# Kernel tuning notes

Hardware: AMD Instinct MI355X
Metric: run time of the kernel (lower is better)

The kernel has to match this reference:

```python
import jax, jax.numpy as jnp
import numpy as np

WS = (7, 7, 7)
DIM = 96
HEADS = 3
NW = 64          # windows per image (mask batch)
BW = 512         # B_ = total windows = 8 images * 64 windows
N = WS[0] * WS[1] * WS[2]  # 343


def _rel_pos_index(ws):
    # Faithful reproduction of the torch buffer (including its multipliers).
    coords = np.stack(np.meshgrid(np.arange(ws[0]), np.arange(ws[1]), np.arange(ws[2]), indexing='ij'))
    cf = coords.reshape(3, -1)                      # [3, N]
    rc = cf[:, :, None] - cf[:, None, :]            # [3, N, N]
    rc = rc.transpose(1, 2, 0).astype(np.int32)     # [N, N, 3]
    rc[:, :, 0] += ws[0] - 1
    rc[:, :, 1] += ws[1] - 1
    rc[:, :, 2] += ws[2] - 1
    rc[:, :, 0] *= 3 * ws[1] - 1
    rc[:, :, 1] *= 2 * ws[1] - 1
    return rc.sum(-1)                               # [N, N]


def setup_inputs() -> dict:
    key = jax.random.key(0)
    ks = jax.random.split(key, 8)
    table_len = (2 * WS[0] - 1) * (2 * WS[1] - 1) * (2 * WS[2] - 1)  # 2197
    x = jax.random.normal(ks[0], (BW, N, DIM), dtype=jnp.float32)
    # shift-window additive mask: 0 where allowed, -100 where masked
    mask = jnp.where(jax.random.uniform(ks[1], (NW, N, N)) < 0.9, 0.0, -100.0).astype(jnp.float32)
    Wqkv = jax.random.normal(ks[2], (3 * DIM, DIM), dtype=jnp.float32) * 0.02
    bqkv = jnp.zeros((3 * DIM,), dtype=jnp.float32)
    Wproj = jax.random.normal(ks[3], (DIM, DIM), dtype=jnp.float32) * 0.02
    bproj = jnp.zeros((DIM,), dtype=jnp.float32)
    logit_scale = jnp.full((HEADS, 1, 1), np.log(10.0), dtype=jnp.float32)
    bias_table = jax.random.normal(ks[4], (table_len, HEADS), dtype=jnp.float32) * 0.02
    rpi = jnp.asarray(_rel_pos_index(WS))           # [N, N] int32
    return {"x": x, "mask": mask, "Wqkv": Wqkv, "bqkv": bqkv,
            "Wproj": Wproj, "bproj": bproj, "logit_scale": logit_scale,
            "bias_table": bias_table, "rpi": rpi}


def reference(x, mask, Wqkv, bqkv, Wproj, bproj, logit_scale, bias_table, rpi):
    B_, Nn, C = x.shape
    H = HEADS
    hd = C // H
    qkv = x @ Wqkv.T + bqkv                          # [B_, N, 3C]
    qkv = qkv.reshape(B_, Nn, 3, H, hd).transpose(2, 0, 3, 1, 4)  # [3, B_, H, N, hd]
    q, k, v = qkv[0], qkv[1], qkv[2]
    # cosine attention: L2-normalize q and k (torch F.normalize, eps=1e-12)
    qn = q / jnp.maximum(jnp.linalg.norm(q, axis=-1, keepdims=True), 1e-12)
    kn = k / jnp.maximum(jnp.linalg.norm(k, axis=-1, keepdims=True), 1e-12)
    attn = jnp.einsum('bhnd,bhmd->bhnm', qn, kn)     # [B_, H, N, N]
    scale = jnp.exp(jnp.minimum(logit_scale, jnp.log(jnp.float32(100.0))))  # [H,1,1]
    attn = attn * scale[None]
    rel_bias = bias_table[rpi.reshape(-1)].reshape(Nn, Nn, H).transpose(2, 0, 1)  # [H, N, N]
    attn = attn + rel_bias[None]
    nW = mask.shape[0]
    attn = attn.reshape(B_ // nW, nW, H, Nn, Nn) + mask[None, :, None]
    attn = attn.reshape(B_, H, Nn, Nn)
    attn = jax.nn.softmax(attn, axis=-1)
    out = jnp.einsum('bhnm,bhmd->bhnd', attn, v)     # [B_, H, N, hd]
    out = out.transpose(0, 2, 1, 3).reshape(B_, Nn, C)
    return out @ Wproj.T + bproj
```

## Files before the change

### kernel.cpp

```cpp
#include <hip/hip_runtime.h>

typedef __attribute__((ext_vector_type(8))) _Float16 half8;
typedef __attribute__((ext_vector_type(4))) _Float16 half4;
typedef __attribute__((ext_vector_type(2))) __fp16 fp16x2;
typedef __attribute__((ext_vector_type(4))) float f32x4;
typedef __attribute__((ext_vector_type(2))) unsigned int uint2v;
typedef __attribute__((ext_vector_type(4))) unsigned int uint4v;

__device__ __forceinline__ _Float16 f2h(float f) { return (_Float16)f; }

#define LOG100 4.605170185988091f
#define LOG2E 1.44269504088896f
#define PADNEG (-100000.0f)

#define MASK_BLOCKS 7744
#define BIAS_BLOCKS 363
__global__ void k_prep(const float* __restrict__ mask, const int* __restrict__ rpi,
                       const float* __restrict__ table,
                       unsigned char* __restrict__ mb, float* __restrict__ bf) {
  if (blockIdx.x < MASK_BLOCKS) {
    int tid = blockIdx.x * 256 + threadIdx.x;
    if (tid >= 64 * 484 * 64) return;
    int lane = tid & 63, idx = tid >> 6;
    int kt = idx % 22, t2 = idx / 22;
    int qt = t2 % 22, w = t2 / 22;
    int R = qt * 16 + (lane & 15), col0 = kt * 16 + (lane >> 4) * 4;
    unsigned bits = 0;
#pragma unroll
    for (int rr = 0; rr < 4; rr++) {
      int col = col0 + rr;
      bool pass = true;
      if (R < 343 && col < 343) pass = mask[((size_t)w * 343 + R) * 343 + col] > -50.f;
      bits |= (pass ? 1u : 0u) << rr;
    }
    mb[tid] = (unsigned char)bits;
  } else {
    int tid = (blockIdx.x - MASK_BLOCKS) * 256 + threadIdx.x;
    if (tid >= 3 * 484 * 64) return;
    int lane = tid & 63, idx = tid >> 6;
    int kt = idx % 22, t2 = idx / 22;
    int qt = t2 % 22, h = t2 / 22;
    int R = qt * 16 + (lane & 15), col0 = kt * 16 + (lane >> 4) * 4;
    f32x4 o;
#pragma unroll
    for (int rr = 0; rr < 4; rr++) {
      int col = col0 + rr;
      o[rr] = (R < 343 && col < 343) ? table[rpi[R * 343 + col] * 3 + h] * LOG2E : PADNEG;
    }
    reinterpret_cast<f32x4*>(bf)[tid] = o;
  }
}

__global__ __launch_bounds__(1024, 1) void k_qkv(
    const float* __restrict__ x, const float* __restrict__ Wqkv,
    const float* __restrict__ bqkv, const float* __restrict__ ls,
    _Float16* __restrict__ q_ws, _Float16* __restrict__ k_ws, _Float16* __restrict__ v_ws) {
  __shared__ alignas(16) _Float16 Wl[288 * 104];
  const int tid = threadIdx.x;
  for (int i = tid; i < 6912; i += 1024) {
    f32x4 w4 = reinterpret_cast<const f32x4*>(Wqkv)[i];
    int f = i * 4, row = f / 96, col = f - row * 96;
    _Float16* dst = &Wl[row * 104 + col];
    dst[0] = f2h(w4[0]); dst[1] = f2h(w4[1]); dst[2] = f2h(w4[2]); dst[3] = f2h(w4[3]);
  }
  __syncthreads();
  const int lane = tid & 63, wv = tid >> 6;
  const int ln15 = lane & 15, quad = lane >> 4;
  const int rowbase = blockIdx.x * 256 + wv * 16;
  const int arow = rowbase + ln15;

  half8 afr[3];
#pragma unroll
  for (int kt = 0; kt < 3; kt++) {
    const float* xp = x + (size_t)arow * 96 + kt * 32 + quad * 8;
    f32x4 a0 = *reinterpret_cast<const f32x4*>(xp);
    f32x4 a1 = *reinterpret_cast<const f32x4*>(xp + 4);
    half8 a;
    a[0] = f2h(a0[0]); a[1] = f2h(a0[1]); a[2] = f2h(a0[2]); a[3] = f2h(a0[3]);
    a[4] = f2h(a1[0]); a[5] = f2h(a1[1]); a[6] = f2h(a1[2]); a[7] = f2h(a1[3]);
    afr[kt] = a;
  }

  int Bb[4], Nn[4];
#pragma unroll
  for (int rr = 0; rr < 4; rr++) {
    int R = rowbase + quad * 4 + rr;
    Bb[rr] = R / 343;
    Nn[rr] = R - Bb[rr] * 343;
  }

  auto ctile = [&](int nt) -> f32x4 {
    f32x4 c = {0.f, 0.f, 0.f, 0.f};
#pragma unroll
    for (int kt = 0; kt < 3; kt++) {
      half8 b = *reinterpret_cast<const half8*>(&Wl[(nt * 16 + ln15) * 104 + kt * 32 + quad * 8]);
      c = __builtin_amdgcn_mfma_f32_16x16x32_f16(afr[kt], b, c, 0, 0, 0);
    }
    return c;
  };

#pragma unroll
  for (int h = 0; h < 3; h++) {
    float sc = __expf(fminf(ls[h], LOG100)) * LOG2E;
    {
      f32x4 c0 = ctile(2 * h), c1 = ctile(2 * h + 1);
      float b0 = bqkv[32 * h + ln15], b1 = bqkv[32 * h + 16 + ln15];
#pragma unroll
      for (int rr = 0; rr < 4; rr++) { c0[rr] += b0; c1[rr] += b1; }
#pragma unroll
      for (int rr = 0; rr < 4; rr++) {
        float s2 = c0[rr] * c0[rr] + c1[rr] * c1[rr];
        s2 += __shfl_xor(s2, 1); s2 += __shfl_xor(s2, 2);
        s2 += __shfl_xor(s2, 4); s2 += __shfl_xor(s2, 8);
        float inv = sc / fmaxf(sqrtf(s2), 1e-12f);
        size_t base = ((size_t)(Bb[rr] * 3 + h) * 343 + Nn[rr]) * 32;
        q_ws[base + ln15] = f2h(c0[rr] * inv);
        q_ws[base + 16 + ln15] = f2h(c1[rr] * inv);
      }
    }
    {
      f32x4 c0 = ctile(6 + 2 * h), c1 = ctile(7 + 2 * h);
      float b0 = bqkv[96 + 32 * h + ln15], b1 = bqkv[96 + 32 * h + 16 + ln15];
#pragma unroll
      for (int rr = 0; rr < 4; rr++) { c0[rr] += b0; c1[rr] += b1; }
#pragma unroll
      for (int rr = 0; rr < 4; rr++) {
        float s2 = c0[rr] * c0[rr] + c1[rr] * c1[rr];
        s2 += __shfl_xor(s2, 1); s2 += __shfl_xor(s2, 2);
        s2 += __shfl_xor(s2, 4); s2 += __shfl_xor(s2, 8);
        float inv = 1.0f / fmaxf(sqrtf(s2), 1e-12f);
        size_t base = ((size_t)(Bb[rr] * 3 + h) * 343 + Nn[rr]) * 32;
        k_ws[base + ln15] = f2h(c0[rr] * inv);
        k_ws[base + 16 + ln15] = f2h(c1[rr] * inv);
      }
    }
    {
      f32x4 c0 = ctile(12 + 2 * h), c1 = ctile(13 + 2 * h);
      float b0 = bqkv[192 + 32 * h + ln15], b1 = bqkv[192 + 32 * h + 16 + ln15];
#pragma unroll
      for (int rr = 0; rr < 4; rr++) {
        size_t base = ((size_t)(Bb[rr] * 3 + h) * 343 + Nn[rr]) * 32;
        v_ws[base + ln15] = f2h(c0[rr] + b0);
        v_ws[base + 16 + ln15] = f2h(c1[rr] + b1);
      }
    }
  }
}

#define KSTR 40
#define VSTR 360
__global__ __launch_bounds__(1024, 8) void k_attn(
    const _Float16* __restrict__ q_ws, const _Float16* __restrict__ k_ws,
    const _Float16* __restrict__ v_ws, const float* __restrict__ bfrag,
    const unsigned char* __restrict__ mb, _Float16* __restrict__ a_ws) {
  __shared__ alignas(16) _Float16 Kl[344 * KSTR];
  __shared__ alignas(16) _Float16 Vt[32 * VSTR];
  const int blk = blockIdx.x;
  const int b = blk / 3, h = blk - b * 3, w = b & 63;
  const size_t slice = (size_t)(b * 3 + h) * 343 * 32;
  const _Float16* qb = q_ws + slice;
  const _Float16* kb = k_ws + slice;
  const _Float16* vb = v_ws + slice;
  const int tid = threadIdx.x, lane = tid & 63, wv = tid >> 6;
  const int ln15 = lane & 15, quad = lane >> 4;

  for (int i = tid; i < 344 * 4; i += 1024) {
    int t = i >> 2, c4 = i & 3;
    half8 kv;
    if (t < 343) kv = *reinterpret_cast<const half8*>(kb + t * 32 + c4 * 8);
    else kv = (half8)(_Float16)0.f;
    *reinterpret_cast<half8*>(&Kl[t * KSTR + c4 * 8]) = kv;
  }
  for (int i = tid; i < 1372; i += 1024) {
    int n = i >> 2, c4 = i & 3;
    half8 vv = *reinterpret_cast<const half8*>(vb + n * 32 + c4 * 8);
#pragma unroll
    for (int j = 0; j < 8; j++) Vt[(c4 * 8 + j) * VSTR + n] = vv[j];
  }
  for (int i = tid; i < 288; i += 1024) {
    int d = i / 9, cc = i - d * 9;
    Vt[d * VSTR + 343 + cc] = (_Float16)0.f;
  }
  __syncthreads();

  const float* bfh = bfrag + (size_t)h * 484 * 64 * 4;
  const unsigned char* mbw = mb + (size_t)w * 484 * 64;
  const fp16x2 kOnes = __builtin_amdgcn_cvt_pkrtz(1.f, 1.f);

#pragma unroll 1
  for (int qt = wv; qt < 22; qt += 16) {
    const int qbase = qt * 16;
    half8 aq = *reinterpret_cast<const half8*>(qb + (size_t)(qbase + ln15) * 32 + quad * 8);
    const f32x4* bq = reinterpret_cast<const f32x4*>(bfh) + (size_t)qt * 22 * 64 + lane;
    const unsigned char* mq = mbw + (size_t)qt * 22 * 64 + lane;

    f32x4 o0 = {0.f, 0.f, 0.f, 0.f}, o1 = {0.f, 0.f, 0.f, 0.f};
    float l00 = 0.f, l01 = 0.f, l10 = 0.f, l11 = 0.f;

    f32x4 ba = bq[0], bb = bq[64];
    unsigned mva = mq[0], mvb = mq[64];
    bq += 128; mq += 128;

#pragma unroll 1
    for (int kc = 0; kc < 11; kc++) {
      int r0 = kc * 32 + ln15;
      int r1 = r0 + 16;
      r1 = (r1 > 343) ? 343 : r1;
      half8 ak0 = *reinterpret_cast<const half8*>(&Kl[r0 * KSTR + quad * 8]);
      half8 ak1 = *reinterpret_cast<const half8*>(&Kl[r1 * KSTR + quad * 8]);
      f32x4 s0 = __builtin_amdgcn_mfma_f32_16x16x32_f16(ak0, aq, ba, 0, 0, 0);
      f32x4 s1 = __builtin_amdgcn_mfma_f32_16x16x32_f16(ak1, aq, bb, 0, 0, 0);

      f32x4 nba = ba, nbb = bb;
      unsigned nmva = mva, nmvb = mvb;
      if (kc < 10) {
        nba = bq[0]; nbb = bq[64];
        nmva = mq[0]; nmvb = mq[64];
        bq += 128; mq += 128;
      }

      float e00 = __builtin_amdgcn_exp2f(s0[0]);
      float e01 = __builtin_amdgcn_exp2f(s0[1]);
      float e02 = __builtin_amdgcn_exp2f(s0[2]);
      float e03 = __builtin_amdgcn_exp2f(s0[3]);
      float e10 = __builtin_amdgcn_exp2f(s1[0]);
      float e11 = __builtin_amdgcn_exp2f(s1[1]);
      float e12 = __builtin_amdgcn_exp2f(s1[2]);
      float e13 = __builtin_amdgcn_exp2f(s1[3]);
      float p00 = ((mva >> 0) & 1u) ? e00 : 0.f;
      float p01 = ((mva >> 1) & 1u) ? e01 : 0.f;
      float p02 = ((mva >> 2) & 1u) ? e02 : 0.f;
      float p03 = ((mva >> 3) & 1u) ? e03 : 0.f;
      float p10 = ((mvb >> 0) & 1u) ? e10 : 0.f;
      float p11 = ((mvb >> 1) & 1u) ? e11 : 0.f;
      float p12 = ((mvb >> 2) & 1u) ? e12 : 0.f;
      float p13 = ((mvb >> 3) & 1u) ? e13 : 0.f;

      fp16x2 w00 = __builtin_amdgcn_cvt_pkrtz(p00, p01);
      fp16x2 w01 = __builtin_amdgcn_cvt_pkrtz(p02, p03);
      fp16x2 w10 = __builtin_amdgcn_cvt_pkrtz(p10, p11);
      fp16x2 w11 = __builtin_amdgcn_cvt_pkrtz(p12, p13);

      l00 = __builtin_amdgcn_fdot2(w00, kOnes, l00, false);
      l01 = __builtin_amdgcn_fdot2(w01, kOnes, l01, false);
      l10 = __builtin_amdgcn_fdot2(w10, kOnes, l10, false);
      l11 = __builtin_amdgcn_fdot2(w11, kOnes, l11, false);

      unsigned a0 = __builtin_bit_cast(unsigned int, w00);
      unsigned a1 = __builtin_bit_cast(unsigned int, w01);
      unsigned b0 = __builtin_bit_cast(unsigned int, w10);
      unsigned b1 = __builtin_bit_cast(unsigned int, w11);
      uint2v r32a = __builtin_amdgcn_permlane32_swap(a0, b0, false, false);
      uint2v r32b = __builtin_amdgcn_permlane32_swap(a1, b1, false, false);
      uint2v r16a = __builtin_amdgcn_permlane16_swap(r32a[0], r32a[1], false, false);
      uint2v r16b = __builtin_amdgcn_permlane16_swap(r32b[0], r32b[1], false, false);
      uint4v pw = {r16a[0], r16b[0], r16a[1], r16b[1]};
      half8 pb = __builtin_bit_cast(half8, pw);

      half8 v0 = *reinterpret_cast<const half8*>(&Vt[ln15 * VSTR + kc * 32 + quad * 8]);
      half8 v1 = *reinterpret_cast<const half8*>(&Vt[(16 + ln15) * VSTR + kc * 32 + quad * 8]);
      o0 = __builtin_amdgcn_mfma_f32_16x16x32_f16(v0, pb, o0, 0, 0, 0);
      o1 = __builtin_amdgcn_mfma_f32_16x16x32_f16(v1, pb, o1, 0, 0, 0);

      ba = nba; bb = nbb; mva = nmva; mvb = nmvb;
    }

    float l = (l00 + l01) + (l10 + l11);
    l += __shfl_xor(l, 16);
    l += __shfl_xor(l, 32);

    const int R = qbase + ln15;
    if (R < 343) {
      float inv = 1.0f / l;
      size_t obase = ((size_t)b * 343 + R) * 96 + h * 32;
      half4 w0, w1;
#pragma unroll
      for (int rr = 0; rr < 4; rr++) {
        w0[rr] = f2h(o0[rr] * inv);
        w1[rr] = f2h(o1[rr] * inv);
      }
      *reinterpret_cast<half4*>(a_ws + obase + quad * 4) = w0;
      *reinterpret_cast<half4*>(a_ws + obase + 16 + quad * 4) = w1;
    }
  }
}

__global__ __launch_bounds__(1024, 1) void k_proj(
    const _Float16* __restrict__ a_ws, const float* __restrict__ Wproj,
    const float* __restrict__ bproj, float* __restrict__ out) {
  __shared__ alignas(16) _Float16 Wl[96 * 104];
  const int tid = threadIdx.x;
  for (int i = tid; i < 2304; i += 1024) {
    f32x4 w4 = reinterpret_cast<const f32x4*>(Wproj)[i];
    int f = i * 4, row = f / 96, col = f - row * 96;
    _Float16* dst = &Wl[row * 104 + col];
    dst[0] = f2h(w4[0]); dst[1] = f2h(w4[1]); dst[2] = f2h(w4[2]); dst[3] = f2h(w4[3]);
  }
  __syncthreads();
  const int lane = tid & 63, wv = tid >> 6;
  const int ln15 = lane & 15, quad = lane >> 4;
  const int rowbase = blockIdx.x * 256 + wv * 16;
  half8 afr[3];
#pragma unroll
  for (int kt = 0; kt < 3; kt++) {
    afr[kt] = *reinterpret_cast<const half8*>(a_ws + (size_t)(rowbase + ln15) * 96 + kt * 32 + quad * 8);
  }
#pragma unroll
  for (int nt = 0; nt < 6; nt++) {
    f32x4 c = {0.f, 0.f, 0.f, 0.f};
#pragma unroll
    for (int kt = 0; kt < 3; kt++) {
      half8 bfr = *reinterpret_cast<const half8*>(&Wl[(nt * 16 + ln15) * 104 + kt * 32 + quad * 8]);
      c = __builtin_amdgcn_mfma_f32_16x16x32_f16(afr[kt], bfr, c, 0, 0, 0);
    }
    float bb = bproj[nt * 16 + ln15];
#pragma unroll
    for (int rr = 0; rr < 4; rr++) {
      int R = rowbase + quad * 4 + rr;
      out[(size_t)R * 96 + nt * 16 + ln15] = c[rr] + bb;
    }
  }
}

extern "C" void kernel_launch(void* const* d_in, const int* in_sizes, int n_in,
                              void* d_out, int out_size, void* d_ws, size_t ws_size,
                              hipStream_t stream) {
  const float* x     = (const float*)d_in[0];
  const float* mask  = (const float*)d_in[1];
  const float* Wqkv  = (const float*)d_in[2];
  const float* bqkv  = (const float*)d_in[3];
  const float* Wproj = (const float*)d_in[4];
  const float* bproj = (const float*)d_in[5];
  const float* ls    = (const float*)d_in[6];
  const float* btab  = (const float*)d_in[7];
  const int*   rpi   = (const int*)d_in[8];
  float* out = (float*)d_out;

  char* ws = (char*)d_ws;
  _Float16* q_ws = (_Float16*)(ws);
  _Float16* k_ws = (_Float16*)(ws + 33718272);
  _Float16* v_ws = (_Float16*)(ws + 67436544);
  _Float16* a_ws = (_Float16*)(ws + 101154816);
  float* bfrag = (float*)(ws + 134873088);
  unsigned char* mbf = (unsigned char*)(ws + 136359936);

  hipLaunchKernelGGL(k_prep, dim3(MASK_BLOCKS + BIAS_BLOCKS), dim3(256), 0, stream,
                     mask, rpi, btab, mbf, bfrag);
  hipLaunchKernelGGL(k_qkv, dim3(686), dim3(1024), 0, stream, x, Wqkv, bqkv, ls, q_ws, k_ws, v_ws);
  hipLaunchKernelGGL(k_attn, dim3(1536), dim3(1024), 0, stream, q_ws, k_ws, v_ws,
                     bfrag, mbf, a_ws);
  hipLaunchKernelGGL(k_proj, dim3(686), dim3(1024), 0, stream, a_ws, Wproj, bproj, out);
}
```

Baseline: 289.7 us.

## Compute softmax row sums via MFMA and precompute fp16 AND-masks for attention

Replaces the per-lane fdot2 row-sum accumulation and cross-lane shuffles with an extra MFMA against a ones matrix, so the denominator comes out already reduced per row. When the workspace is large enough, the prep kernel expands the mask into 16-bit all-ones/zero words laid out per 32-column chunk. A new attention kernel applies the mask with a bitwise AND on packed fp16 probabilities instead of per-element selects. This trades more mask memory traffic (16 bytes per lane per chunk instead of 1 byte) and an extra MFMA per chunk for fewer VALU operations.

```diff
diff --git a/kernel.cpp b/kernel.cpp
--- a/kernel.cpp
+++ b/kernel.cpp
@@ -15,25 +15,53 @@
 
 #define MASK_BLOCKS 7744
 #define BIAS_BLOCKS 363
+#define WS_BIG_END 152219648ull
+
 __global__ void k_prep(const float* __restrict__ mask, const int* __restrict__ rpi,
-                       const float* __restrict__ table,
-                       unsigned char* __restrict__ mb, float* __restrict__ bf) {
+                       const float* __restrict__ table, unsigned char* __restrict__ mb,
+                       uint4v* __restrict__ mand, float* __restrict__ bf, int big) {
   if (blockIdx.x < MASK_BLOCKS) {
-    int tid = blockIdx.x * 256 + threadIdx.x;
-    if (tid >= 64 * 484 * 64) return;
-    int lane = tid & 63, idx = tid >> 6;
-    int kt = idx % 22, t2 = idx / 22;
-    int qt = t2 % 22, w = t2 / 22;
-    int R = qt * 16 + (lane & 15), col0 = kt * 16 + (lane >> 4) * 4;
-    unsigned bits = 0;
-#pragma unroll
-    for (int rr = 0; rr < 4; rr++) {
-      int col = col0 + rr;
-      bool pass = true;
-      if (R < 343 && col < 343) pass = mask[((size_t)w * 343 + R) * 343 + col] > -50.f;
-      bits |= (pass ? 1u : 0u) << rr;
-    }
-    mb[tid] = (unsigned char)bits;
+    if (big) {
+      int tid = blockIdx.x * 256 + threadIdx.x;
+      if (tid >= 64 * 22 * 11 * 64) return;
+      int lane = tid & 63, idx = tid >> 6;
+      int kc = idx % 11, t2 = idx / 11;
+      int qt = t2 % 22, w = t2 / 22;
+      int R = qt * 16 + (lane & 15), col0 = (lane >> 4) * 4;
+      unsigned wd[4];
+#pragma unroll
+      for (int j = 0; j < 2; j++) {
+        int kt = kc * 2 + j;
+        unsigned bits[4];
+#pragma unroll
+        for (int rr = 0; rr < 4; rr++) {
+          int col = kt * 16 + col0 + rr;
+          bool pass = true;
+          if (R < 343 && col < 343) pass = mask[((size_t)w * 343 + R) * 343 + col] > -50.f;
+          bits[rr] = pass ? 0xFFFFu : 0u;
+        }
+        wd[j * 2] = bits[0] | (bits[1] << 16);
+        wd[j * 2 + 1] = bits[2] | (bits[3] << 16);
+      }
+      uint4v o = {wd[0], wd[1], wd[2], wd[3]};
+      mand[tid] = o;
+    } else {
+      int tid = blockIdx.x * 256 + threadIdx.x;
+      if (tid >= 64 * 484 * 64) return;
+      int lane = tid & 63, idx = tid >> 6;
+      int kt = idx % 22, t2 = idx / 22;
+      int qt = t2 % 22, w = t2 / 22;
+      int R = qt * 16 + (lane & 15), col0 = kt * 16 + (lane >> 4) * 4;
+      unsigned bits = 0;
+#pragma unroll
+      for (int rr = 0; rr < 4; rr++) {
+        int col = col0 + rr;
+        bool pass = true;
+        if (R < 343 && col < 343) pass = mask[((size_t)w * 343 + R) * 343 + col] > -50.f;
+        bits |= (pass ? 1u : 0u) << rr;
+      }
+      mb[tid] = (unsigned char)bits;
+    }
   } else {
     int tid = (blockIdx.x - MASK_BLOCKS) * 256 + threadIdx.x;
     if (tid >= 3 * 484 * 64) return;
@@ -149,6 +177,127 @@
 
 #define KSTR 40
 #define VSTR 360
+
+__global__ __launch_bounds__(1024, 8) void k_attn_big(
+    const _Float16* __restrict__ q_ws, const _Float16* __restrict__ k_ws,
+    const _Float16* __restrict__ v_ws, const float* __restrict__ bfrag,
+    const uint4v* __restrict__ mand, _Float16* __restrict__ a_ws) {
+  __shared__ alignas(16) _Float16 Kl[344 * KSTR];
+  __shared__ alignas(16) _Float16 Vt[32 * VSTR];
+  const int blk = blockIdx.x;
+  const int b = blk / 3, h = blk - b * 3, w = b & 63;
+  const size_t slice = (size_t)(b * 3 + h) * 343 * 32;
+  const _Float16* qb = q_ws + slice;
+  const _Float16* kb = k_ws + slice;
+  const _Float16* vb = v_ws + slice;
+  const int tid = threadIdx.x, lane = tid & 63, wv = tid >> 6;
+  const int ln15 = lane & 15, quad = lane >> 4;
+
+  for (int i = tid; i < 344 * 4; i += 1024) {
+    int t = i >> 2, c4 = i & 3;
+    half8 kv;
+    if (t < 343) kv = *reinterpret_cast<const half8*>(kb + t * 32 + c4 * 8);
+    else kv = (half8)(_Float16)0.f;
+    *reinterpret_cast<half8*>(&Kl[t * KSTR + c4 * 8]) = kv;
+  }
+  for (int i = tid; i < 1372; i += 1024) {
+    int n = i >> 2, c4 = i & 3;
+    half8 vv = *reinterpret_cast<const half8*>(vb + n * 32 + c4 * 8);
+#pragma unroll
+    for (int j = 0; j < 8; j++) Vt[(c4 * 8 + j) * VSTR + n] = vv[j];
+  }
+  for (int i = tid; i < 288; i += 1024) {
+    int d = i / 9, cc = i - d * 9;
+    Vt[d * VSTR + 343 + cc] = (_Float16)0.f;
+  }
+  __syncthreads();
+
+  const float* bfh = bfrag + (size_t)h * 484 * 64 * 4;
+  half8 ones8;
+#pragma unroll
+  for (int j = 0; j < 8; j++) ones8[j] = (_Float16)1.f;
+
+#pragma unroll 1
+  for (int qt = wv; qt < 22; qt += 16) {
+    const int qbase = qt * 16;
+    half8 aq = *reinterpret_cast<const half8*>(qb + (size_t)(qbase + ln15) * 32 + quad * 8);
+    const f32x4* bq = reinterpret_cast<const f32x4*>(bfh) + (size_t)qt * 22 * 64 + lane;
+    const uint4v* mq = mand + ((size_t)w * 22 + qt) * 11 * 64 + lane;
+
+    f32x4 o0 = {0.f, 0.f, 0.f, 0.f}, o1 = {0.f, 0.f, 0.f, 0.f};
+    f32x4 lacc = {0.f, 0.f, 0.f, 0.f};
+
+    f32x4 ba = bq[0], bb = bq[64];
+    uint4v mw = mq[0];
+    bq += 128; mq += 64;
+
+#pragma unroll 1
+    for (int kc = 0; kc < 11; kc++) {
+      int r0 = kc * 32 + ln15;
+      int r1 = r0 + 16;
+      r1 = (r1 > 343) ? 343 : r1;
+      half8 ak0 = *reinterpret_cast<const half8*>(&Kl[r0 * KSTR + quad * 8]);
+      half8 ak1 = *reinterpret_cast<const half8*>(&Kl[r1 * KSTR + quad * 8]);
+      f32x4 s0 = __builtin_amdgcn_mfma_f32_16x16x32_f16(ak0, aq, ba, 0, 0, 0);
+      f32x4 s1 = __builtin_amdgcn_mfma_f32_16x16x32_f16(ak1, aq, bb, 0, 0, 0);
+
+      f32x4 nba = ba, nbb = bb;
+      uint4v nmw = mw;
+      if (kc < 10) {
+        nba = bq[0]; nbb = bq[64]; nmw = mq[0];
+        bq += 128; mq += 64;
+      }
+
+      float p00 = __builtin_amdgcn_exp2f(s0[0]);
+      float p01 = __builtin_amdgcn_exp2f(s0[1]);
+      float p02 = __builtin_amdgcn_exp2f(s0[2]);
+      float p03 = __builtin_amdgcn_exp2f(s0[3]);
+      float p10 = __builtin_amdgcn_exp2f(s1[0]);
+      float p11 = __builtin_amdgcn_exp2f(s1[1]);
+      float p12 = __builtin_amdgcn_exp2f(s1[2]);
+      float p13 = __builtin_amdgcn_exp2f(s1[3]);
+
+      fp16x2 w00 = __builtin_amdgcn_cvt_pkrtz(p00, p01);
+      fp16x2 w01 = __builtin_amdgcn_cvt_pkrtz(p02, p03);
+      fp16x2 w10 = __builtin_amdgcn_cvt_pkrtz(p10, p11);
+      fp16x2 w11 = __builtin_amdgcn_cvt_pkrtz(p12, p13);
+      unsigned a0 = __builtin_bit_cast(unsigned int, w00) & mw[0];
+      unsigned a1 = __builtin_bit_cast(unsigned int, w01) & mw[1];
+      unsigned b0 = __builtin_bit_cast(unsigned int, w10) & mw[2];
+      unsigned b1 = __builtin_bit_cast(unsigned int, w11) & mw[3];
+
+      uint2v r32a = __builtin_amdgcn_permlane32_swap(a0, b0, false, false);
+      uint2v r32b = __builtin_amdgcn_permlane32_swap(a1, b1, false, false);
+      uint2v r16a = __builtin_amdgcn_permlane16_swap(r32a[0], r32a[1], false, false);
+      uint2v r16b = __builtin_amdgcn_permlane16_swap(r32b[0], r32b[1], false, false);
+      uint4v pw = {r16a[0], r16b[0], r16a[1], r16b[1]};
+      half8 pb = __builtin_bit_cast(half8, pw);
+
+      half8 v0 = *reinterpret_cast<const half8*>(&Vt[ln15 * VSTR + kc * 32 + quad * 8]);
+      half8 v1 = *reinterpret_cast<const half8*>(&Vt[(16 + ln15) * VSTR + kc * 32 + quad * 8]);
+      o0 = __builtin_amdgcn_mfma_f32_16x16x32_f16(v0, pb, o0, 0, 0, 0);
+      o1 = __builtin_amdgcn_mfma_f32_16x16x32_f16(v1, pb, o1, 0, 0, 0);
+      lacc = __builtin_amdgcn_mfma_f32_16x16x32_f16(ones8, pb, lacc, 0, 0, 0);
+
+      ba = nba; bb = nbb; mw = nmw;
+    }
+
+    const int R = qbase + ln15;
+    if (R < 343) {
+      float inv = 1.0f / lacc[0];
+      size_t obase = ((size_t)b * 343 + R) * 96 + h * 32;
+      half4 w0, w1;
+#pragma unroll
+      for (int rr = 0; rr < 4; rr++) {
+        w0[rr] = f2h(o0[rr] * inv);
+        w1[rr] = f2h(o1[rr] * inv);
+      }
+      *reinterpret_cast<half4*>(a_ws + obase + quad * 4) = w0;
+      *reinterpret_cast<half4*>(a_ws + obase + 16 + quad * 4) = w1;
+    }
+  }
+}
+
 __global__ __launch_bounds__(1024, 8) void k_attn(
     const _Float16* __restrict__ q_ws, const _Float16* __restrict__ k_ws,
     const _Float16* __restrict__ v_ws, const float* __restrict__ bfrag,
@@ -185,7 +334,9 @@
 
   const float* bfh = bfrag + (size_t)h * 484 * 64 * 4;
   const unsigned char* mbw = mb + (size_t)w * 484 * 64;
-  const fp16x2 kOnes = __builtin_amdgcn_cvt_pkrtz(1.f, 1.f);
+  half8 ones8;
+#pragma unroll
+  for (int j = 0; j < 8; j++) ones8[j] = (_Float16)1.f;
 
 #pragma unroll 1
   for (int qt = wv; qt < 22; qt += 16) {
@@ -195,7 +346,7 @@
     const unsigned char* mq = mbw + (size_t)qt * 22 * 64 + lane;
 
     f32x4 o0 = {0.f, 0.f, 0.f, 0.f}, o1 = {0.f, 0.f, 0.f, 0.f};
-    float l00 = 0.f, l01 = 0.f, l10 = 0.f, l11 = 0.f;
+    f32x4 lacc = {0.f, 0.f, 0.f, 0.f};
 
     f32x4 ba = bq[0], bb = bq[64];
     unsigned mva = mq[0], mvb = mq[64];
@@ -241,11 +392,6 @@
       fp16x2 w10 = __builtin_amdgcn_cvt_pkrtz(p10, p11);
       fp16x2 w11 = __builtin_amdgcn_cvt_pkrtz(p12, p13);
 
-      l00 = __builtin_amdgcn_fdot2(w00, kOnes, l00, false);
-      l01 = __builtin_amdgcn_fdot2(w01, kOnes, l01, false);
-      l10 = __builtin_amdgcn_fdot2(w10, kOnes, l10, false);
-      l11 = __builtin_amdgcn_fdot2(w11, kOnes, l11, false);
-
       unsigned a0 = __builtin_bit_cast(unsigned int, w00);
       unsigned a1 = __builtin_bit_cast(unsigned int, w01);
       unsigned b0 = __builtin_bit_cast(unsigned int, w10);
@@ -261,17 +407,14 @@
       half8 v1 = *reinterpret_cast<const half8*>(&Vt[(16 + ln15) * VSTR + kc * 32 + quad * 8]);
       o0 = __builtin_amdgcn_mfma_f32_16x16x32_f16(v0, pb, o0, 0, 0, 0);
       o1 = __builtin_amdgcn_mfma_f32_16x16x32_f16(v1, pb, o1, 0, 0, 0);
+      lacc = __builtin_amdgcn_mfma_f32_16x16x32_f16(ones8, pb, lacc, 0, 0, 0);
 
       ba = nba; bb = nbb; mva = nmva; mvb = nmvb;
     }
-
-    float l = (l00 + l01) + (l10 + l11);
-    l += __shfl_xor(l, 16);
-    l += __shfl_xor(l, 32);
 
     const int R = qbase + ln15;
     if (R < 343) {
-      float inv = 1.0f / l;
+      float inv = 1.0f / lacc[0];
       size_t obase = ((size_t)b * 343 + R) * 96 + h * 32;
       half4 w0, w1;
 #pragma unroll
@@ -343,11 +486,18 @@
   _Float16* a_ws = (_Float16*)(ws + 101154816);
   float* bfrag = (float*)(ws + 134873088);
   unsigned char* mbf = (unsigned char*)(ws + 136359936);
+  uint4v* mand = (uint4v*)(ws + 136359936);
+  const int big = (ws_size >= WS_BIG_END) ? 1 : 0;
 
   hipLaunchKernelGGL(k_prep, dim3(MASK_BLOCKS + BIAS_BLOCKS), dim3(256), 0, stream,
-                     mask, rpi, btab, mbf, bfrag);
+                     mask, rpi, btab, mbf, mand, bfrag, big);
   hipLaunchKernelGGL(k_qkv, dim3(686), dim3(1024), 0, stream, x, Wqkv, bqkv, ls, q_ws, k_ws, v_ws);
-  hipLaunchKernelGGL(k_attn, dim3(1536), dim3(1024), 0, stream, q_ws, k_ws, v_ws,
-                     bfrag, mbf, a_ws);
+  if (big) {
+    hipLaunchKernelGGL(k_attn_big, dim3(1536), dim3(1024), 0, stream, q_ws, k_ws, v_ws,
+                       bfrag, mand, a_ws);
+  } else {
+    hipLaunchKernelGGL(k_attn, dim3(1536), dim3(1024), 0, stream, q_ws, k_ws, v_ws,
+                       bfrag, mbf, a_ws);
+  }
   hipLaunchKernelGGL(k_proj, dim3(686), dim3(1024), 0, stream, a_ws, Wproj, bproj, out);
 }
```

Result: no change. 293.1 us (+1.2%).
